# Optimization experiments

Hardware: AMD Instinct MI355X
Metric: run time of the kernel (lower is better)

The kernel has to match this reference:

```python
import jax, jax.numpy as jnp
import numpy as np


def setup_inputs() -> dict:
    key = jax.random.key(0)
    bs, n_heads, ch, length = 4, 8, 64, 2048
    width = 3 * n_heads * ch  # 1536
    qkv = jax.random.normal(key, (bs, width, length), dtype=jnp.float32)
    return {"qkv": qkv, "n_heads": n_heads}


def reference(qkv, n_heads):
    bs, width, length = qkv.shape
    ch = width // (3 * n_heads)
    # reshape to (bs*heads, 3*ch, length) then split into q, k, v of (B, ch, L)
    qkv_r = qkv.reshape(bs * n_heads, 3 * ch, length)
    q, k, v = qkv_r[:, :ch], qkv_r[:, ch:2 * ch], qkv_r[:, 2 * ch:]
    scale = ch ** (-0.5)
    # weight = bmm(q^T, k) * scale -> (B, L_q, L_k)
    weight = jnp.einsum('bct,bcs->bts', q, k) * scale
    weight = jax.nn.softmax(weight.astype(jnp.float32), axis=-1).astype(qkv.dtype)
    # a = bmm(v, weight^T) -> (B, ch, L)
    a = jnp.einsum('bcs,bts->bct', v, weight)
    return a.reshape(bs, n_heads * ch, length)
```

## Files before the change

### kernel.cpp

```cpp
#include <hip/hip_runtime.h>

typedef __bf16 bf16;
typedef __attribute__((ext_vector_type(8)))  __bf16 bf16x8;
typedef __attribute__((ext_vector_type(16))) float  f32x16;

#define LEN   2048
#define CH    64
#define HEADS 32

union PackU { unsigned u[4]; bf16x8 v; };

static __device__ inline unsigned pack2(float lo, float hi) {
  union { bf16 h[2]; unsigned u; } p;
  p.h[0] = (bf16)lo; p.h[1] = (bf16)hi;
  return p.u;
}

__global__ __launch_bounds__(256) void prep_kernel(const float* __restrict__ qkv,
                                                   bf16* __restrict__ ws) {
  __shared__ float tile[64][65];
  const int tIdx = blockIdx.x;
  const int g    = blockIdx.y;
  const int tid  = threadIdx.x;
  const int s0   = tIdx * 64;
  const float* K = qkv + (g * 192 + 64)  * LEN;
  const float* V = qkv + (g * 192 + 128) * LEN;

  {
    const int c0 = tid >> 6, s = tid & 63;
#pragma unroll
    for (int i = 0; i < 16; ++i) {
      const int c = c0 + i * 4;
      tile[c][s] = K[c * LEN + s0 + s];
    }
  }
  __syncthreads();

  bf16* dst = ws + ((size_t)g * 32 + tIdx) * 8192;
#pragma unroll
  for (int it = 0; it < 2; ++it) {
    const int c2 = tid + it * 256;
    const int r  = c2 >> 6, ln = c2 & 63;
    const int nn = ln & 31, hh = ln >> 5;
    const int kb = r >> 1,  mb = r & 1;
    const int s  = mb * 32 + nn;
    const int cg = kb * 2 + hh;
    bf16x8 o;
#pragma unroll
    for (int j = 0; j < 8; ++j) o[j] = (bf16)tile[cg * 8 + j][s];
    *(bf16x8*)(dst + c2 * 8) = o;
  }
#pragma unroll
  for (int it = 0; it < 2; ++it) {
    const int c2  = tid + it * 256;
    const int r   = c2 >> 6, ln = c2 & 63;
    const int nn  = ln & 31, hh = ln >> 5;
    const int kbs = r >> 1,  mbo = r & 1;
    const int k8  = kbs * 2 + hh;
    const int pa  = 32 * (k8 >> 2) + 8 * ((k8 >> 1) & 1) + 4 * (k8 & 1);
    const float* src = V + (mbo * 32 + nn) * LEN + s0 + pa;
    const float4 a = *(const float4*)src;
    const float4 b = *(const float4*)(src + 16);
    bf16x8 o;
    o[0] = (bf16)a.x; o[1] = (bf16)a.y; o[2] = (bf16)a.z; o[3] = (bf16)a.w;
    o[4] = (bf16)b.x; o[5] = (bf16)b.y; o[6] = (bf16)b.z; o[7] = (bf16)b.w;
    *(bf16x8*)(dst + 4096 + c2 * 8) = o;
  }
}

__global__ __launch_bounds__(512, 2) void attn_kernel(const float* __restrict__ qkv,
                                                      const bf16* __restrict__ ws,
                                                      float* __restrict__ out) {
  __shared__ __align__(16) float fx[9344];

  const int tid  = threadIdx.x;
  const int lane = tid & 63;
  const int w    = tid >> 6;
  const int wv   = w & 3;
  const int sg   = w >> 2;
  const int n    = lane & 31;
  const int h    = lane >> 5;
  const int g    = blockIdx.x & 31;
  const int jb   = blockIdx.x >> 5;
  const int t0   = jb * 128 + wv * 32;

  const bf16* wsg = ws + (size_t)g * (32 * 8192);

  const float qs = 0.125f * 1.44269504088896340736f;
  const float* Q = qkv + g * (192 * LEN);
  bf16x8 qf[4];
#pragma unroll
  for (int kb = 0; kb < 4; ++kb)
#pragma unroll
    for (int jj = 0; jj < 8; ++jj)
      qf[kb][jj] = (bf16)(Q[(kb * 16 + h * 8 + jj) * LEN + t0 + n] * qs);

  f32x16 o_acc[2];
#pragma unroll
  for (int mb = 0; mb < 2; ++mb)
#pragma unroll
    for (int r = 0; r < 16; ++r) o_acc[mb][r] = 0.f;
  float l_acc = 0.f;

  f32x16 zf;
#pragma unroll
  for (int r = 0; r < 16; ++r) zf[r] = 0.f;

  for (int it = 0; it < 16; ++it) {
    const int i = 2 * it + sg;
    const bf16* tb = wsg + i * 8192;

    bf16x8 ka[8], vf[8];
#pragma unroll
    for (int r = 0; r < 8; ++r)
      ka[r] = *(const bf16x8*)(tb + r * 512 + lane * 8);
#pragma unroll
    for (int r = 0; r < 8; ++r)
      vf[r] = *(const bf16x8*)(tb + 4096 + r * 512 + lane * 8);

    f32x16 sf[2];
    __builtin_amdgcn_s_setprio(1);
#pragma unroll
    for (int mb = 0; mb < 2; ++mb)
      sf[mb] = __builtin_amdgcn_mfma_f32_32x32x16_bf16(ka[mb], qf[0], zf, 0, 0, 0);
#pragma unroll
    for (int kb = 1; kb < 4; ++kb)
#pragma unroll
      for (int mb = 0; mb < 2; ++mb)
        sf[mb] = __builtin_amdgcn_mfma_f32_32x32x16_bf16(ka[kb * 2 + mb], qf[kb], sf[mb], 0, 0, 0);
    __builtin_amdgcn_s_setprio(0);

    PackU frag[4];
    float ls = 0.f;
#pragma unroll
    for (int mb = 0; mb < 2; ++mb)
#pragma unroll
      for (int u = 0; u < 4; ++u) {
        const float p0 = __builtin_amdgcn_exp2f(sf[mb][4 * u + 0]);
        const float p1 = __builtin_amdgcn_exp2f(sf[mb][4 * u + 1]);
        const float p2 = __builtin_amdgcn_exp2f(sf[mb][4 * u + 2]);
        const float p3 = __builtin_amdgcn_exp2f(sf[mb][4 * u + 3]);
        ls += (p0 + p1) + (p2 + p3);
        const int kb   = 2 * mb + (u & 1);
        const int base = 2 * (u >> 1);
        frag[kb].u[base]     = pack2(p0, p1);
        frag[kb].u[base + 1] = pack2(p2, p3);
      }
    l_acc += ls;

    __builtin_amdgcn_s_setprio(1);
#pragma unroll
    for (int kbs = 0; kbs < 4; ++kbs)
#pragma unroll
      for (int mbo = 0; mbo < 2; ++mbo)
        o_acc[mbo] = __builtin_amdgcn_mfma_f32_32x32x16_bf16(vf[kbs * 2 + mbo], frag[kbs].v, o_acc[mbo], 0, 0, 0);
    __builtin_amdgcn_s_setprio(0);
  }

  float lt = l_acc + __shfl_xor(l_acc, 32);
  float* lx = fx + 9216;

  __syncthreads();
  if (sg == 1) {
#pragma unroll
    for (int mbo = 0; mbo < 2; ++mbo)
#pragma unroll
      for (int u = 0; u < 4; ++u) {
        float4 st;
        st.x = o_acc[mbo][4 * u + 0];
        st.y = o_acc[mbo][4 * u + 1];
        st.z = o_acc[mbo][4 * u + 2];
        st.w = o_acc[mbo][4 * u + 3];
        *(float4*)&fx[wv * 2304 + lane * 36 + mbo * 16 + 4 * u] = st;
      }
    if (h == 0) lx[wv * 32 + n] = lt;
  }
  __syncthreads();
  if (sg == 0) {
    const float inv = 1.0f / (lt + lx[wv * 32 + n]);
    float* og = out + g * (CH * LEN);
#pragma unroll
    for (int mbo = 0; mbo < 2; ++mbo)
#pragma unroll
      for (int u = 0; u < 4; ++u) {
        const float4 q = *(const float4*)&fx[wv * 2304 + lane * 36 + mbo * 16 + 4 * u];
#pragma unroll
        for (int j = 0; j < 4; ++j) {
          const int r = 4 * u + j;
          const int c = 32 * mbo + (r & 3) + 8 * (r >> 2) + 4 * h;
          og[c * LEN + t0 + n] = (o_acc[mbo][r] + ((const float*)&q)[j]) * inv;
        }
      }
  }
}

extern "C" void kernel_launch(void* const* d_in, const int* in_sizes, int n_in,
                              void* d_out, int out_size, void* d_ws, size_t ws_size,
                              hipStream_t stream) {
  const float* qkv = (const float*)d_in[0];
  float* out = (float*)d_out;
  bf16* ws = (bf16*)d_ws;

  prep_kernel<<<dim3(32, HEADS), 256, 0, stream>>>(qkv, ws);
  attn_kernel<<<dim3(512), 512, 0, stream>>>(qkv, ws, out);
}
```

Measured before the change: 130.4 us.

## Software-pipeline attention loop: overlap PV MFMA with next tile's loads and exp

Restructures the main attention loop into a prologue, a steady-state loop and an epilogue. Each iteration's PV MFMAs run on the previous tile's probabilities while the next tile's K and V fragments are loaded and its QK^T and exp are computed. The intent is to hide global-load latency and interleave MFMA with the VALU exp work. Launch bounds also drop from 2 to 1 blocks per CU to give the extra live registers room, which lowers occupancy.

```diff
diff --git a/kernel.cpp b/kernel.cpp
--- a/kernel.cpp
+++ b/kernel.cpp
@@ -68,7 +68,7 @@
   }
 }
 
-__global__ __launch_bounds__(512, 2) void attn_kernel(const float* __restrict__ qkv,
+__global__ __launch_bounds__(512, 1) void attn_kernel(const float* __restrict__ qkv,
                                                       const bf16* __restrict__ ws,
                                                       float* __restrict__ out) {
   __shared__ __align__(16) float fx[9344];
@@ -106,17 +106,14 @@
 #pragma unroll
   for (int r = 0; r < 16; ++r) zf[r] = 0.f;
 
-  for (int it = 0; it < 16; ++it) {
-    const int i = 2 * it + sg;
-    const bf16* tb = wsg + i * 8192;
-
-    bf16x8 ka[8], vf[8];
+  bf16x8 ka[8], vf[8];
+  PackU  frag[4];
+
+  {
+    const bf16* tb = wsg + sg * 8192;
 #pragma unroll
     for (int r = 0; r < 8; ++r)
       ka[r] = *(const bf16x8*)(tb + r * 512 + lane * 8);
-#pragma unroll
-    for (int r = 0; r < 8; ++r)
-      vf[r] = *(const bf16x8*)(tb + 4096 + r * 512 + lane * 8);
 
     f32x16 sf[2];
     __builtin_amdgcn_s_setprio(1);
@@ -130,7 +127,10 @@
         sf[mb] = __builtin_amdgcn_mfma_f32_32x32x16_bf16(ka[kb * 2 + mb], qf[kb], sf[mb], 0, 0, 0);
     __builtin_amdgcn_s_setprio(0);
 
-    PackU frag[4];
+#pragma unroll
+    for (int r = 0; r < 8; ++r)
+      vf[r] = *(const bf16x8*)(tb + 4096 + r * 512 + lane * 8);
+
     float ls = 0.f;
 #pragma unroll
     for (int mb = 0; mb < 2; ++mb)
@@ -147,6 +147,15 @@
         frag[kb].u[base + 1] = pack2(p2, p3);
       }
     l_acc += ls;
+  }
+
+  for (int it = 1; it < 16; ++it) {
+    const int i = 2 * it + sg;
+    const bf16* tb = wsg + i * 8192;
+
+#pragma unroll
+    for (int r = 0; r < 8; ++r)
+      ka[r] = *(const bf16x8*)(tb + r * 512 + lane * 8);
 
     __builtin_amdgcn_s_setprio(1);
 #pragma unroll
@@ -155,7 +164,48 @@
       for (int mbo = 0; mbo < 2; ++mbo)
         o_acc[mbo] = __builtin_amdgcn_mfma_f32_32x32x16_bf16(vf[kbs * 2 + mbo], frag[kbs].v, o_acc[mbo], 0, 0, 0);
     __builtin_amdgcn_s_setprio(0);
-  }
+
+#pragma unroll
+    for (int r = 0; r < 8; ++r)
+      vf[r] = *(const bf16x8*)(tb + 4096 + r * 512 + lane * 8);
+
+    f32x16 sf[2];
+    __builtin_amdgcn_s_setprio(1);
+#pragma unroll
+    for (int mb = 0; mb < 2; ++mb)
+      sf[mb] = __builtin_amdgcn_mfma_f32_32x32x16_bf16(ka[mb], qf[0], zf, 0, 0, 0);
+#pragma unroll
+    for (int kb = 1; kb < 4; ++kb)
+#pragma unroll
+      for (int mb = 0; mb < 2; ++mb)
+        sf[mb] = __builtin_amdgcn_mfma_f32_32x32x16_bf16(ka[kb * 2 + mb], qf[kb], sf[mb], 0, 0, 0);
+    __builtin_amdgcn_s_setprio(0);
+
+    float ls = 0.f;
+#pragma unroll
+    for (int mb = 0; mb < 2; ++mb)
+#pragma unroll
+      for (int u = 0; u < 4; ++u) {
+        const float p0 = __builtin_amdgcn_exp2f(sf[mb][4 * u + 0]);
+        const float p1 = __builtin_amdgcn_exp2f(sf[mb][4 * u + 1]);
+        const float p2 = __builtin_amdgcn_exp2f(sf[mb][4 * u + 2]);
+        const float p3 = __builtin_amdgcn_exp2f(sf[mb][4 * u + 3]);
+        ls += (p0 + p1) + (p2 + p3);
+        const int kb   = 2 * mb + (u & 1);
+        const int base = 2 * (u >> 1);
+        frag[kb].u[base]     = pack2(p0, p1);
+        frag[kb].u[base + 1] = pack2(p2, p3);
+      }
+    l_acc += ls;
+  }
+
+  __builtin_amdgcn_s_setprio(1);
+#pragma unroll
+  for (int kbs = 0; kbs < 4; ++kbs)
+#pragma unroll
+    for (int mbo = 0; mbo < 2; ++mbo)
+      o_acc[mbo] = __builtin_amdgcn_mfma_f32_32x32x16_bf16(vf[kbs * 2 + mbo], frag[kbs].v, o_acc[mbo], 0, 0, 0);
+  __builtin_amdgcn_s_setprio(0);
 
   float lt = l_acc + __shfl_xor(l_acc, 32);
   float* lx = fx + 9216;
```

After: 133.4 us. 1.02x slower.
